# Performance work log

Hardware: AMD Instinct MI355X
Metric: run time of the kernel (lower is better)

## Reference

```python
import jax, jax.numpy as jnp
import numpy as np

N = 50000        # num nodes
E = 1_000_000    # num edges
F_IN = 256       # input feature dim
UNITS = 128      # hidden units
NUM_CLASSES = 40 # output classes
EPS = 1e-3       # Keras BatchNormalization default epsilon


def setup_inputs() -> dict:
    key = jax.random.key(0)
    ks = jax.random.split(key, 32)
    inp = {
        "x": jax.random.normal(ks[0], (N, F_IN), jnp.float32),
        "edge_index": jax.random.randint(ks[1], (2, E), 0, N, jnp.int32),
        "edge_weight": jax.random.uniform(ks[2], (E,), jnp.float32),
    }
    dims = [(F_IN, UNITS), (UNITS, UNITS), (UNITS, NUM_CLASSES)]
    ki = 3
    for li, (fi, fo) in enumerate(dims, 1):
        inp[f"w_gcn{li}"] = jax.random.normal(ks[ki], (fi, fo), jnp.float32) / np.sqrt(fi).astype(np.float32); ki += 1
        inp[f"w_self{li}"] = jax.random.normal(ks[ki], (fi, fo), jnp.float32) / np.sqrt(fi).astype(np.float32); ki += 1
        inp[f"b{li}"] = jnp.zeros((fo,), jnp.float32)
        inp[f"gamma{li}"] = 1.0 + 0.1 * jax.random.normal(ks[ki], (fo,), jnp.float32); ki += 1
        inp[f"beta{li}"] = 0.1 * jax.random.normal(ks[ki], (fo,), jnp.float32); ki += 1
        inp[f"mean{li}"] = 0.1 * jax.random.normal(ks[ki], (fo,), jnp.float32); ki += 1
        inp[f"var{li}"] = jnp.ones((fo,), jnp.float32)
    return inp


def _gcn_bs(h, src, dst, norm_w, w_gcn, w_self, b, gamma, beta, mean, var, act):
    # GCN aggregation: transform then gather->weight->scatter-sum
    hw = h @ w_gcn                                   # [N, out]
    msg = hw[src] * norm_w[:, None]                  # [E, out]
    agg = jax.ops.segment_sum(msg, dst, num_segments=N)
    out = agg + h @ w_self + b                       # self-loop dense + bias
    # BatchNorm (inference: moving stats)
    out = (out - mean) * jax.lax.rsqrt(var + EPS) * gamma + beta
    return act(out) if act is not None else out


def reference(x, edge_index, edge_weight,
              w_gcn1, w_self1, b1, gamma1, beta1, mean1, var1,
              w_gcn2, w_self2, b2, gamma2, beta2, mean2, var2,
              w_gcn3, w_self3, b3, gamma3, beta3, mean3, var3):
    src, dst = edge_index[0], edge_index[1]
    # symmetric GCN normalization (renorm=False: no added self loops)
    deg = jax.ops.segment_sum(edge_weight, dst, num_segments=N)
    dinv = jnp.where(deg > 0, jax.lax.rsqrt(jnp.where(deg > 0, deg, 1.0)), 0.0)
    norm_w = dinv[src] * edge_weight * dinv[dst]
    # inference: DropEdge and Dropout are identity
    h = _gcn_bs(x, src, dst, norm_w, w_gcn1, w_self1, b1, gamma1, beta1, mean1, var1, jax.nn.relu)
    h = _gcn_bs(h, src, dst, norm_w, w_gcn2, w_self2, b2, gamma2, beta2, mean2, var2, jax.nn.relu)
    h = _gcn_bs(h, src, dst, norm_w, w_gcn3, w_self3, b3, gamma3, beta3, mean3, var3, None)
    return h
```

## Files before the change

### kernel.cpp

```cpp
#include <hip/hip_runtime.h>
#include <hip/hip_bf16.h>

#define NN 50000
#define EE 1000000
static constexpr float EPSV = 1e-3f;
static constexpr float FIXSCALE = 16777216.f;

typedef __attribute__((ext_vector_type(8))) short short8;
typedef __attribute__((ext_vector_type(4))) float fx4;

__device__ inline float blo(unsigned u) { return __uint_as_float(u << 16); }
__device__ inline float bhi(unsigned u) { return __uint_as_float(u & 0xffff0000u); }
__device__ inline unsigned short f2b(float f) {
    __hip_bfloat16 h = __float2bfloat16(f);
    return *(unsigned short*)&h;
}
__device__ inline unsigned pack2(float a, float b) {
    return (unsigned)f2b(a) | ((unsigned)f2b(b) << 16);
}

__device__ inline void gload_lds16(const unsigned short* g, unsigned short* ldsbase) {
    __builtin_amdgcn_global_load_lds(
        (const __attribute__((address_space(1))) unsigned int*)(const void*)g,
        (__attribute__((address_space(3))) unsigned int*)(void*)ldsbase, 16, 0, 0);
}


#define ZB 3125
#define WB1 256
#define WB2 128
#define WB3 64

__global__ void setup_kernel(float* __restrict__ zp,
                             const float* __restrict__ wg1, const float* __restrict__ ws1,
                             unsigned short* __restrict__ Wt1,
                             const float* __restrict__ wg2, const float* __restrict__ ws2,
                             unsigned short* __restrict__ Wt2,
                             const float* __restrict__ wg3, const float* __restrict__ ws3,
                             unsigned short* __restrict__ Wt3) {
    int b = blockIdx.x;
    int t = threadIdx.x;
    if (b < ZB) {
        int i = b * 256 + t;
        if (i < 800000) zp[i] = 0.f;
    } else if (b < ZB + WB1) {
        int idx = (b - ZB) * 256 + t;
        int n = idx >> 8, k = idx & 255;
        float v = (n < 128) ? wg1[(size_t)k * 128 + n]
                            : ws1[(size_t)k * 128 + (n - 128)];
        Wt1[idx] = f2b(v);
    } else if (b < ZB + WB1 + WB2) {
        int idx = (b - ZB - WB1) * 256 + t;
        int n = idx >> 7, k = idx & 127;
        float v = (n < 128) ? wg2[(size_t)k * 128 + n]
                            : ws2[(size_t)k * 128 + (n - 128)];
        Wt2[idx] = f2b(v);
    } else {
        int idx = (b - ZB - WB1 - WB2) * 256 + t;
        int n = idx >> 7, k = idx & 127;
        float v = 0.f;
        if (n < 40) v = wg3[(size_t)k * 40 + n];
        else if (n < 80) v = ws3[(size_t)k * 40 + (n - 40)];
        Wt3[idx] = f2b(v);
    }
}


#define CBH 1954
#define XBH 6250

__global__ void preA_kernel(const int* __restrict__ ei, const float* __restrict__ ew,
                            unsigned long long* __restrict__ cnt64p, unsigned* __restrict__ rank,
                            const float4* __restrict__ x, uint2* __restrict__ xb) {
    int b = blockIdx.x;
    int t = threadIdx.x;
    if (b < CBH) {
        int e = b * 256 + t;
        if (e < 500000) {
            int d = ei[EE + e];
            unsigned fx = __float2uint_rn(ew[e] * FIXSCALE);
            unsigned long long old =
                atomicAdd(&cnt64p[(size_t)d << 3], 0x100000000ull | (unsigned long long)fx);
            rank[e] = (unsigned)(old >> 32);
        }
    } else {
        int i = (b - CBH) * 256 + t;
        float4 v = x[i];
        xb[i] = make_uint2(pack2(v.x, v.y), pack2(v.z, v.w));
    }
}

__global__ void preB_kernel(const int* __restrict__ ei, const float* __restrict__ ew,
                            unsigned long long* __restrict__ cnt64p, unsigned* __restrict__ rank,
                            const float4* __restrict__ x, uint2* __restrict__ xb) {
    int b = blockIdx.x;
    int t = threadIdx.x;
    if (b < CBH) {
        int e = 500000 + b * 256 + t;
        if (e < EE) {
            int d = ei[EE + e];
            unsigned fx = __float2uint_rn(ew[e] * FIXSCALE);
            unsigned long long old =
                atomicAdd(&cnt64p[(size_t)d << 3], 0x100000000ull | (unsigned long long)fx);
            rank[e] = (unsigned)(old >> 32);
        }
    } else {
        int i = 1600000 + (b - CBH) * 256 + t;
        float4 v = x[i];
        xb[i] = make_uint2(pack2(v.x, v.y), pack2(v.z, v.w));
    }
}


__global__ __launch_bounds__(1024) void dinvsum_kernel(const unsigned long long* __restrict__ cnt64p,
                                                       float* __restrict__ dinv,
                                                       int* __restrict__ bsum) {
    __shared__ int s[1024];
    const int t = threadIdx.x;
    int idx = blockIdx.x * 1024 + t;
    unsigned long long cv = 0ull;
    if (idx < NN) cv = cnt64p[(size_t)idx << 3];
    float deg = (float)(unsigned)cv * (1.f / FIXSCALE);
    if (idx < NN) dinv[idx] = (deg > 0.f) ? rsqrtf(deg) : 0.f;
    s[t] = (int)(unsigned)(cv >> 32);
    __syncthreads();
#pragma unroll
    for (int off = 512; off > 0; off >>= 1) {
        if (t < off) s[t] += s[t + off];
        __syncthreads();
    }
    if (t == 0) bsum[blockIdx.x] = s[0];
}

__global__ __launch_bounds__(64) void scanB_kernel(const int* __restrict__ bsum,
                                                   int* __restrict__ bpre, int nb) {
    int t = threadIdx.x;
    int v = (t < nb) ? bsum[t] : 0;
    int own = v;
#pragma unroll
    for (int off = 1; off < 64; off <<= 1) {
        int u = __shfl_up(v, off);
        if (t >= off) v += u;
    }
    if (t < nb) bpre[t] = v - own;
}

__global__ __launch_bounds__(1024) void scanC_kernel(const unsigned long long* __restrict__ cnt64p,
                                                     const int* __restrict__ bpre,
                                                     int* __restrict__ rowstart) {
    __shared__ int s[1024];
    const int t = threadIdx.x;
    int idx = blockIdx.x * 1024 + t;
    int v = (idx < NN) ? (int)(unsigned)(cnt64p[(size_t)idx << 3] >> 32) : 0;
    s[t] = v;
    __syncthreads();
#pragma unroll
    for (int off = 1; off < 1024; off <<= 1) {
        int u = (t >= off) ? s[t - off] : 0;
        __syncthreads();
        s[t] += u;
        __syncthreads();
    }
    if (idx < NN) rowstart[idx] = s[t] - v + bpre[blockIdx.x];
    if (idx == 0) rowstart[NN] = EE;
}

__global__ void fill_kernel(const int* __restrict__ ei, const float* __restrict__ ew,
                            const float* __restrict__ dinv, const int* __restrict__ rowstart,
                            const unsigned* __restrict__ rank, unsigned* __restrict__ eprec4) {
    int e = blockIdx.x * blockDim.x + threadIdx.x;
    if (e >= EE) return;
    int s = ei[e], d = ei[EE + e];
    int idx = rowstart[d] + (int)rank[e];
    float w = dinv[s] * ew[e] * dinv[d];
    eprec4[idx] = ((unsigned)s << 16) | (unsigned)f2b(w);
}


__global__ __launch_bounds__(256) void gemm_mfma(const unsigned short* __restrict__ Ab,
                                                 const unsigned short* __restrict__ Wt,
                                                 const float* __restrict__ bias,
                                                 unsigned short* __restrict__ Cg,
                                                 unsigned short* __restrict__ Cs,
                                                 int M, int K, int Fo) {
    __shared__ unsigned short sA[128 * 64];
    __shared__ unsigned short sB[128 * 64];

    const int t = threadIdx.x;
    const int lane = t & 63;
    const int wave = t >> 6;
    const int wm = wave >> 1, wn = wave & 1;
    const int l15 = lane & 15, quad = lane >> 4;
    const int row0 = blockIdx.x * 128;
    const int colbase = blockIdx.y * 128;

    fx4 acc[4][4];
#pragma unroll
    for (int r = 0; r < 4; ++r)
#pragma unroll
        for (int c = 0; c < 4; ++c) acc[r][c] = (fx4){0.f, 0.f, 0.f, 0.f};

    for (int kc = 0; kc < K; kc += 64) {
#pragma unroll
        for (int j = 0; j < 4; ++j) {
            int c = wave * 4 + j;
            int rb = c >> 1, kh = c & 1;
            int ar = row0 + rb * 16 + l15;
            if (ar >= M) ar = M - 1;
            int ak = kc + kh * 32 + quad * 8;
            gload_lds16(Ab + (size_t)ar * K + ak, sA + c * 512);
            int br = colbase + rb * 16 + l15;
            gload_lds16(Wt + (size_t)br * K + ak, sB + c * 512);
        }
        __syncthreads();

#pragma unroll
        for (int kh = 0; kh < 2; ++kh) {
            short8 a[4], b[4];
#pragma unroll
            for (int r = 0; r < 4; ++r)
                a[r] = *reinterpret_cast<const short8*>(&sA[((wm * 4 + r) * 2 + kh) * 512 + lane * 8]);
#pragma unroll
            for (int c = 0; c < 4; ++c)
                b[c] = *reinterpret_cast<const short8*>(&sB[((wn * 4 + c) * 2 + kh) * 512 + lane * 8]);
#pragma unroll
            for (int r = 0; r < 4; ++r)
#pragma unroll
                for (int c = 0; c < 4; ++c)
                    acc[r][c] = __builtin_amdgcn_mfma_f32_16x16x32_bf16(a[r], b[c], acc[r][c], 0, 0, 0);
        }
        __syncthreads();
    }

#pragma unroll
    for (int c = 0; c < 4; ++c) {
        int f = colbase + wn * 64 + c * 16 + l15;
        if (f >= 2 * Fo) continue;
        bool isG = (f < Fo);
        int col = isG ? f : f - Fo;
        float badd = isG ? 0.f : bias[col];
        unsigned short* base = isG ? Cg : Cs;
#pragma unroll
        for (int r = 0; r < 4; ++r) {
#pragma unroll
            for (int reg = 0; reg < 4; ++reg) {
                int row = row0 + wm * 64 + r * 16 + quad * 4 + reg;
                if (row < M) base[(size_t)row * Fo + col] = f2b(acc[r][c][reg] + badd);
            }
        }
    }
}


template <bool RELU>
__global__ __launch_bounds__(256) void agg128_kernel(
    const int* __restrict__ rowstart, const unsigned* __restrict__ eprec4,
    const unsigned* __restrict__ hw, const unsigned* __restrict__ selfC,
    const float* __restrict__ g, const float* __restrict__ be,
    const float* __restrict__ mu, const float* __restrict__ va,
    unsigned* __restrict__ out) {
    int wave = threadIdx.x >> 6;
    int lane = threadIdx.x & 63;
    int n = blockIdx.x * 4 + wave;
    if (n >= NN) return;
    unsigned scp = selfC[n * 64 + lane];
    float acc0 = blo(scp), acc1 = bhi(scp);
    int beg = rowstart[n], end = rowstart[n + 1];
    int i = beg;
    for (; i + 4 <= end; i += 4) {
        unsigned e0 = eprec4[i], e1 = eprec4[i + 1], e2 = eprec4[i + 2], e3 = eprec4[i + 3];
        unsigned v0 = hw[(e0 >> 16) * 64u + lane];
        unsigned v1 = hw[(e1 >> 16) * 64u + lane];
        unsigned v2 = hw[(e2 >> 16) * 64u + lane];
        unsigned v3 = hw[(e3 >> 16) * 64u + lane];
        float w0 = blo(e0), w1 = blo(e1), w2 = blo(e2), w3 = blo(e3);
        acc0 += blo(v0) * w0; acc1 += bhi(v0) * w0;
        acc0 += blo(v1) * w1; acc1 += bhi(v1) * w1;
        acc0 += blo(v2) * w2; acc1 += bhi(v2) * w2;
        acc0 += blo(v3) * w3; acc1 += bhi(v3) * w3;
    }
    for (; i < end; ++i) {
        unsigned e = eprec4[i];
        unsigned v = hw[(e >> 16) * 64u + lane];
        float w = blo(e);
        acc0 += blo(v) * w; acc1 += bhi(v) * w;
    }
    float2 m2 = reinterpret_cast<const float2*>(mu)[lane];
    float2 v2f = reinterpret_cast<const float2*>(va)[lane];
    float2 g2 = reinterpret_cast<const float2*>(g)[lane];
    float2 b2 = reinterpret_cast<const float2*>(be)[lane];
    float r0 = (acc0 - m2.x) * rsqrtf(v2f.x + EPSV) * g2.x + b2.x;
    float r1 = (acc1 - m2.y) * rsqrtf(v2f.y + EPSV) * g2.y + b2.y;
    if (RELU) {
        r0 = fmaxf(r0, 0.f);
        r1 = fmaxf(r1, 0.f);
    }
    out[n * 64 + lane] = pack2(r0, r1);
}


__global__ __launch_bounds__(256) void agg40_kernel(
    const int* __restrict__ rowstart, const unsigned* __restrict__ eprec4,
    const unsigned* __restrict__ hw, const unsigned* __restrict__ selfC,
    const float* __restrict__ g, const float* __restrict__ be,
    const float* __restrict__ mu, const float* __restrict__ va,
    float* __restrict__ out) {
    int wave = threadIdx.x >> 6;
    int lane = threadIdx.x & 63;
    int n = blockIdx.x * 4 + wave;
    if (n >= NN) return;
    int grp = lane / 20;
    int fl = lane - grp * 20;
    float acc0 = 0.f, acc1 = 0.f;
    int beg = rowstart[n], end = rowstart[n + 1];
    if (grp < 3) {
        for (int i = beg + grp; i < end; i += 3) {
            unsigned e = eprec4[i];
            unsigned v = hw[(e >> 16) * 20u + fl];
            float w = blo(e);
            acc0 += blo(v) * w;
            acc1 += bhi(v) * w;
        }
    }
    acc0 += __shfl(acc0, lane + 20) + __shfl(acc0, lane + 40);
    acc1 += __shfl(acc1, lane + 20) + __shfl(acc1, lane + 40);
    if (lane < 20) {
        int f0 = lane * 2;
        unsigned scp = selfC[n * 20 + lane];
        acc0 += blo(scp);
        acc1 += bhi(scp);
        float2 m2 = reinterpret_cast<const float2*>(mu)[lane];
        float2 v2f = reinterpret_cast<const float2*>(va)[lane];
        float2 g2 = reinterpret_cast<const float2*>(g)[lane];
        float2 b2 = reinterpret_cast<const float2*>(be)[lane];
        float r0 = (acc0 - m2.x) * rsqrtf(v2f.x + EPSV) * g2.x + b2.x;
        float r1 = (acc1 - m2.y) * rsqrtf(v2f.y + EPSV) * g2.y + b2.y;
        *reinterpret_cast<float2*>(&out[(size_t)n * 40 + f0]) = make_float2(r0, r1);
    }
}


extern "C" void kernel_launch(void* const* d_in, const int* in_sizes, int n_in,
                              void* d_out, int out_size, void* d_ws, size_t ws_size,
                              hipStream_t stream) {
    const float* x = (const float*)d_in[0];
    const int* ei = (const int*)d_in[1];
    const float* ew = (const float*)d_in[2];

    const float* wg[3]  = {(const float*)d_in[3],  (const float*)d_in[10], (const float*)d_in[17]};
    const float* wsf[3] = {(const float*)d_in[4],  (const float*)d_in[11], (const float*)d_in[18]};
    const float* bs[3]  = {(const float*)d_in[5],  (const float*)d_in[12], (const float*)d_in[19]};
    const float* gm[3]  = {(const float*)d_in[6],  (const float*)d_in[13], (const float*)d_in[20]};
    const float* bt[3]  = {(const float*)d_in[7],  (const float*)d_in[14], (const float*)d_in[21]};
    const float* mu[3]  = {(const float*)d_in[8],  (const float*)d_in[15], (const float*)d_in[22]};
    const float* vr[3]  = {(const float*)d_in[9],  (const float*)d_in[16], (const float*)d_in[23]};

    float* W = (float*)d_ws;
    float* dinv     = W + 100096;
    unsigned* rank  = (unsigned*)(W + 150144);
    int*   bsum     = (int*)(W + 1150144);
    int*   bpre     = (int*)(W + 1150208);
    int*   rowstart = (int*)(W + 1150272);
    unsigned* eprec4 = (unsigned*)(W + 1200384);
    unsigned short* Wt1 = (unsigned short*)(W + 2200384);
    unsigned short* Wt2 = (unsigned short*)(W + 2233152);
    unsigned short* Wt3 = (unsigned short*)(W + 2249536);
    unsigned short* xb  = (unsigned short*)(W + 2257728);
    unsigned short* bufH = (unsigned short*)(W + 2257728);
    unsigned short* bufHW = (unsigned short*)(W + 8657728);
    unsigned short* bufSb = (unsigned short*)(W + 11857728);
    unsigned long long* cnt64p = (unsigned long long*)(W + 11857728);

    const int B = 256;
    const int SB = 49;

    setup_kernel<<<ZB + WB1 + WB2 + WB3, B, 0, stream>>>(
        (float*)cnt64p, wg[0], wsf[0], Wt1, wg[1], wsf[1], Wt2, wg[2], wsf[2], Wt3);

    preA_kernel<<<CBH + XBH, B, 0, stream>>>(ei, ew, cnt64p, rank, (const float4*)x, (uint2*)xb);
    preB_kernel<<<CBH + XBH, B, 0, stream>>>(ei, ew, cnt64p, rank, (const float4*)x, (uint2*)xb);

    dinvsum_kernel<<<SB, 1024, 0, stream>>>(cnt64p, dinv, bsum);
    scanB_kernel<<<1, 64, 0, stream>>>(bsum, bpre, SB);
    scanC_kernel<<<SB, 1024, 0, stream>>>(cnt64p, bpre, rowstart);
    fill_kernel<<<(EE + B - 1) / B, B, 0, stream>>>(ei, ew, dinv, rowstart, rank, eprec4);

    const int aggGrid = (NN + 3) / 4;
    dim3 g2((NN + 127) / 128, 2), g1((NN + 127) / 128, 1);

    gemm_mfma<<<g2, B, 0, stream>>>(xb, Wt1, bs[0], bufHW, bufSb, NN, 256, 128);
    agg128_kernel<true><<<aggGrid, B, 0, stream>>>(rowstart, eprec4, (const unsigned*)bufHW,
                                                   (const unsigned*)bufSb, gm[0], bt[0], mu[0], vr[0],
                                                   (unsigned*)bufH);

    gemm_mfma<<<g2, B, 0, stream>>>(bufH, Wt2, bs[1], bufHW, bufSb, NN, 128, 128);
    agg128_kernel<true><<<aggGrid, B, 0, stream>>>(rowstart, eprec4, (const unsigned*)bufHW,
                                                   (const unsigned*)bufSb, gm[1], bt[1], mu[1], vr[1],
                                                   (unsigned*)bufH);

    gemm_mfma<<<g1, B, 0, stream>>>(bufH, Wt3, bs[2], bufHW, bufSb, NN, 128, 40);
    agg40_kernel<<<aggGrid, B, 0, stream>>>(rowstart, eprec4, (const unsigned*)bufHW,
                                            (const unsigned*)bufSb, gm[2], bt[2], mu[2], vr[2],
                                            (float*)d_out);
}
```

Before: 428.9 us.

## Software-pipeline edge gathers in aggregation kernels and shrink counter zeroing

The 128-wide aggregation kernel now processes edges in batches of eight and prefetches the next batch's edge records while the current gathers are in flight. It uses a wave-uniform (readfirstlane) base index so the record loads can be scalar. The 40-wide kernel unrolls its strided edge loop by four to raise memory-level parallelism. Setup now zeroes only one 64-bit counter every 8 elements (one per node) instead of clearing 800k floats. That assumes the other words in the counter region need no zeroing, and the extra registers may reduce occupancy.

```diff
diff --git a/kernel.cpp b/kernel.cpp
--- a/kernel.cpp
+++ b/kernel.cpp
@@ -26,12 +26,12 @@
 }
 
 
-#define ZB 3125
+#define ZB 196
 #define WB1 256
 #define WB2 128
 #define WB3 64
 
-__global__ void setup_kernel(float* __restrict__ zp,
+__global__ void setup_kernel(unsigned long long* __restrict__ cnt64p,
                              const float* __restrict__ wg1, const float* __restrict__ ws1,
                              unsigned short* __restrict__ Wt1,
                              const float* __restrict__ wg2, const float* __restrict__ ws2,
@@ -42,7 +42,7 @@
     int t = threadIdx.x;
     if (b < ZB) {
         int i = b * 256 + t;
-        if (i < 800000) zp[i] = 0.f;
+        if (i < NN) cnt64p[(size_t)i << 3] = 0ull;
     } else if (b < ZB + WB1) {
         int idx = (b - ZB) * 256 + t;
         int n = idx >> 8, k = idx & 255;
@@ -267,6 +267,44 @@
     float acc0 = blo(scp), acc1 = bhi(scp);
     int beg = rowstart[n], end = rowstart[n + 1];
     int i = beg;
+
+    if (i + 8 <= end) {
+        unsigned e[8];
+        {
+            int ifl = __builtin_amdgcn_readfirstlane(i);
+#pragma unroll
+            for (int k = 0; k < 8; ++k) e[k] = eprec4[ifl + k];
+        }
+        for (; i + 16 <= end; i += 8) {
+            unsigned v[8];
+#pragma unroll
+            for (int k = 0; k < 8; ++k) v[k] = hw[(e[k] >> 16) * 64u + lane];
+            unsigned en[8];
+            {
+                int ifl = __builtin_amdgcn_readfirstlane(i + 8);
+#pragma unroll
+                for (int k = 0; k < 8; ++k) en[k] = eprec4[ifl + k];
+            }
+#pragma unroll
+            for (int k = 0; k < 8; ++k) {
+                float w = blo(e[k]);
+                acc0 += blo(v[k]) * w;
+                acc1 += bhi(v[k]) * w;
+            }
+#pragma unroll
+            for (int k = 0; k < 8; ++k) e[k] = en[k];
+        }
+        unsigned v[8];
+#pragma unroll
+        for (int k = 0; k < 8; ++k) v[k] = hw[(e[k] >> 16) * 64u + lane];
+#pragma unroll
+        for (int k = 0; k < 8; ++k) {
+            float w = blo(e[k]);
+            acc0 += blo(v[k]) * w;
+            acc1 += bhi(v[k]) * w;
+        }
+        i += 8;
+    }
     for (; i + 4 <= end; i += 4) {
         unsigned e0 = eprec4[i], e1 = eprec4[i + 1], e2 = eprec4[i + 2], e3 = eprec4[i + 3];
         unsigned v0 = hw[(e0 >> 16) * 64u + lane];
@@ -314,7 +352,20 @@
     float acc0 = 0.f, acc1 = 0.f;
     int beg = rowstart[n], end = rowstart[n + 1];
     if (grp < 3) {
-        for (int i = beg + grp; i < end; i += 3) {
+        int i = beg + grp;
+        for (; i + 9 < end; i += 12) {
+            unsigned e0 = eprec4[i], e1 = eprec4[i + 3], e2 = eprec4[i + 6], e3 = eprec4[i + 9];
+            unsigned v0 = hw[(e0 >> 16) * 20u + fl];
+            unsigned v1 = hw[(e1 >> 16) * 20u + fl];
+            unsigned v2 = hw[(e2 >> 16) * 20u + fl];
+            unsigned v3 = hw[(e3 >> 16) * 20u + fl];
+            float w0 = blo(e0), w1 = blo(e1), w2 = blo(e2), w3 = blo(e3);
+            acc0 += blo(v0) * w0; acc1 += bhi(v0) * w0;
+            acc0 += blo(v1) * w1; acc1 += bhi(v1) * w1;
+            acc0 += blo(v2) * w2; acc1 += bhi(v2) * w2;
+            acc0 += blo(v3) * w3; acc1 += bhi(v3) * w3;
+        }
+        for (; i < end; i += 3) {
             unsigned e = eprec4[i];
             unsigned v = hw[(e >> 16) * 20u + fl];
             float w = blo(e);
@@ -375,7 +426,7 @@
     const int SB = 49;
 
     setup_kernel<<<ZB + WB1 + WB2 + WB3, B, 0, stream>>>(
-        (float*)cnt64p, wg[0], wsf[0], Wt1, wg[1], wsf[1], Wt2, wg[2], wsf[2], Wt3);
+        cnt64p, wg[0], wsf[0], Wt1, wg[1], wsf[1], Wt2, wg[2], wsf[2], Wt3);
 
     preA_kernel<<<CBH + XBH, B, 0, stream>>>(ei, ew, cnt64p, rank, (const float4*)x, (uint2*)xb);
     preB_kernel<<<CBH + XBH, B, 0, stream>>>(ei, ew, cnt64p, rank, (const float4*)x, (uint2*)xb);
```

New measurement: 394.6 us. -8.0%, faster.
